# Kernel optimization log

Measured on AMD Instinct MI355X. Metric: run time of the kernel, lower is better.

## Reference

```python
import jax, jax.numpy as jnp
import numpy as np

B, T, D, H = 512, 1024, 64, 64     # batch, time, input_size, hidden_size
R = 4                              # number of reward heads
MH = 32                            # MLP hidden size


def setup_inputs() -> dict:
    key = jax.random.key(0)
    ks = jax.random.split(key, 16)
    s = lambda k, shape, scale=1.0: jax.random.normal(k, shape, dtype=jnp.float32) * scale
    inp = {
        "x": s(ks[0], (B, T, D)),
        # learned initial states (nn.Parameter randn(1,1,H) -> store as (H,))
        "h_init": s(ks[1], (H,)),
        "c_init": s(ks[2], (H,)),
        # LSTM params, PyTorch layout: W_ih (4H, D), W_hh (4H, H), gate order i,f,g,o
        "W_ih": s(ks[3], (4 * H, D), 1.0 / np.sqrt(H)),
        "W_hh": s(ks[4], (4 * H, H), 1.0 / np.sqrt(H)),
        "b_ih": s(ks[5], (4 * H,), 1.0 / np.sqrt(H)),
        "b_hh": s(ks[6], (4 * H,), 1.0 / np.sqrt(H)),
        # R stacked MLP heads: Linear(H,MH) -> ReLU -> Linear(MH,MH) -> ReLU -> Linear(MH,1)
        "W1": s(ks[7], (R, MH, H), 1.0 / np.sqrt(H)),
        "b1": s(ks[8], (R, MH), 1.0 / np.sqrt(H)),
        "W2": s(ks[9], (R, MH, MH), 1.0 / np.sqrt(MH)),
        "b2": s(ks[10], (R, MH), 1.0 / np.sqrt(MH)),
        "W3": s(ks[11], (R, 1, MH), 1.0 / np.sqrt(MH)),
        "b3": s(ks[12], (R, 1), 1.0 / np.sqrt(MH)),
    }
    return inp


def _lstm(x, h0, c0, W_ih, W_hh, b_ih, b_hh):
    # x: (B, T, D). Returns y: (B, T, H).
    Hh = h0.shape[-1]
    b = b_ih + b_hh                      # (4H,)
    # precompute input projections for all steps: (T, B, 4H)
    xg = jnp.einsum('btd,gd->tbg', x, W_ih) + b

    def step(carry, xg_t):
        h, c = carry                     # (B, H) each
        gates = xg_t + h @ W_hh.T        # (B, 4H)
        i, f, g, o = jnp.split(gates, 4, axis=-1)
        c = jax.nn.sigmoid(f) * c + jax.nn.sigmoid(i) * jnp.tanh(g)
        h = jax.nn.sigmoid(o) * jnp.tanh(c)
        return (h, c), h

    Bb = x.shape[0]
    h0b = jnp.broadcast_to(h0, (Bb, Hh))
    c0b = jnp.broadcast_to(c0, (Bb, Hh))
    _, ys = jax.lax.scan(step, (h0b, c0b), xg)   # ys: (T, B, H)
    return jnp.transpose(ys, (1, 0, 2))


def _heads(y, W1, b1, W2, b2, W3, b3):
    # y: (B, T, H) -> (R, B, T); all R heads computed in one batched einsum chain
    h1 = jax.nn.relu(jnp.einsum('bth,rmh->rbtm', y, W1) + b1[:, None, None, :])
    h2 = jax.nn.relu(jnp.einsum('rbtm,rnm->rbtn', h1, W2) + b2[:, None, None, :])
    out = jnp.einsum('rbtn,ron->rbto', h2, W3) + b3[:, None, None, :]
    return out[..., 0]                   # squeeze last dim -> (R, B, T)


def reference(x, h_init, c_init, W_ih, W_hh, b_ih, b_hh, W1, b1, W2, b2, W3, b3):
    y = _lstm(x, h_init, c_init, W_ih, W_hh, b_ih, b_hh)
    outs = _heads(y, W1, b1, W2, b2, W3, b3)   # (R, B, T); row r == rewards[r] head
    return (y, outs)
```

## Files before the change

kernel.cpp:

```cpp
#include <hip/hip_runtime.h>

#define BB 512
#define TT 1024
#define DD 64
#define HH 64
#define G4 256
#define RR 4
#define MHH 32
#define BT (BB * TT)
#define Y_SIZE (BB * TT * HH)

typedef _Float16 half8 __attribute__((ext_vector_type(8)));
typedef _Float16 half4 __attribute__((ext_vector_type(4)));
typedef float f32x4 __attribute__((ext_vector_type(4)));

#define MFMA16(a, b, c) __builtin_amdgcn_mfma_f32_16x16x32_f16((a), (b), (c), 0, 0, 0)

__device__ __forceinline__ float sigm(float x) {
    return __builtin_amdgcn_rcpf(1.0f + __expf(-x));
}
__device__ __forceinline__ float tanh_(float x) {
    return 1.0f - 2.0f * __builtin_amdgcn_rcpf(1.0f + __expf(2.0f * x));
}

__device__ __forceinline__ half8 cvt8(f32x4 a, f32x4 b) {
    half8 h;
    h[0] = (_Float16)a[0]; h[1] = (_Float16)a[1];
    h[2] = (_Float16)a[2]; h[3] = (_Float16)a[3];
    h[4] = (_Float16)b[0]; h[5] = (_Float16)b[1];
    h[6] = (_Float16)b[2]; h[7] = (_Float16)b[3];
    return h;
}

__global__ __launch_bounds__(256) void lstm_kernel(
    const float* __restrict__ x, const float* __restrict__ h_init,
    const float* __restrict__ c_init, const float* __restrict__ W_ih,
    const float* __restrict__ W_hh, const float* __restrict__ b_ih,
    const float* __restrict__ b_hh, float* __restrict__ y)
{
    __shared__ alignas(16) _Float16 xch[2][16][2][DD];
    __shared__ alignas(16) _Float16 hst[2][2][HH];

    const int tid  = threadIdx.x;
    const int wave = tid >> 6;
    const int lane = tid & 63;
    const int col  = lane & 15;
    const int quad = lane >> 4;
    const int sel  = (lane >> 3) & 1;
    const int r_act = lane >> 5;
    const int j    = (wave << 4) + col;
    const bool writer = ((lane >> 4) & 1) == 0;

    const int b0 = blockIdx.x * 2;

    half8 bf[4][4];
    float bias[4];
#pragma unroll
    for (int G = 0; G < 4; ++G) {
        const int n = (G << 6) + j;
        bias[G] = b_ih[n] + b_hh[n];
#pragma unroll
        for (int c = 0; c < 4; ++c) {
            const float* src = (c < 2) ? (W_ih + n * DD + c * 32 + quad * 8)
                                       : (W_hh + n * HH + (c - 2) * 32 + quad * 8);
            f32x4 w0 = *(const f32x4*)src;
            f32x4 w1 = *(const f32x4*)(src + 4);
            bf[G][c] = cvt8(w0, w1);
        }
    }

    float c_state = c_init[j];

    if (tid < 128) {
        const int rr = tid >> 6, jj = tid & 63;
        hst[0][rr][jj] = (_Float16)h_init[jj];
    }
    {
        const int ss = tid >> 4, rr = (tid >> 3) & 1, j0 = (tid & 7) << 3;
        const float* src = x + ((b0 + rr) * TT + ss) * DD + j0;
        f32x4 g0 = *(const f32x4*)src;
        f32x4 g1 = *(const f32x4*)(src + 4);
        *(half8*)&xch[0][ss][rr][j0] = cvt8(g0, g1);
    }
    __syncthreads();

    const int ss_pf = tid >> 4, rr_pf = (tid >> 3) & 1, j0_pf = (tid & 7) << 3;

    for (int ci = 0; ci < 64; ++ci) {
        const int buf = ci & 1;
        const bool pf = (ci + 1) < 64;
        f32x4 g0, g1;
        if (pf) {
            const float* src = x + ((b0 + rr_pf) * TT + ((ci + 1) << 4) + ss_pf) * DD + j0_pf;
            g0 = *(const f32x4*)src;
            g1 = *(const f32x4*)(src + 4);
        }
#pragma unroll
        for (int s = 0; s < 16; ++s) {
            const int t = (ci << 4) + s;
            const int p = s & 1;
            const _Float16* xrow = &xch[buf][s][sel][0];
            half8 a0 = *(const half8*)(xrow + quad * 8);
            half8 a1 = *(const half8*)(xrow + 32 + quad * 8);
            const _Float16* hrow = &hst[p][sel][0];
            half8 a2 = *(const half8*)(hrow + quad * 8);
            half8 a3 = *(const half8*)(hrow + 32 + quad * 8);

            f32x4 acc0 = {bias[0], bias[0], bias[0], bias[0]};
            f32x4 acc1 = {bias[1], bias[1], bias[1], bias[1]};
            f32x4 acc2 = {bias[2], bias[2], bias[2], bias[2]};
            f32x4 acc3 = {bias[3], bias[3], bias[3], bias[3]};
            acc0 = MFMA16(a0, bf[0][0], acc0); acc0 = MFMA16(a1, bf[0][1], acc0);
            acc0 = MFMA16(a2, bf[0][2], acc0); acc0 = MFMA16(a3, bf[0][3], acc0);
            acc1 = MFMA16(a0, bf[1][0], acc1); acc1 = MFMA16(a1, bf[1][1], acc1);
            acc1 = MFMA16(a2, bf[1][2], acc1); acc1 = MFMA16(a3, bf[1][3], acc1);
            acc2 = MFMA16(a0, bf[2][0], acc2); acc2 = MFMA16(a1, bf[2][1], acc2);
            acc2 = MFMA16(a2, bf[2][2], acc2); acc2 = MFMA16(a3, bf[2][3], acc2);
            acc3 = MFMA16(a0, bf[3][0], acc3); acc3 = MFMA16(a1, bf[3][1], acc3);
            acc3 = MFMA16(a2, bf[3][2], acc3); acc3 = MFMA16(a3, bf[3][3], acc3);

            const float si = sigm(acc0[0]);
            const float sf = sigm(acc1[0]);
            const float tg = tanh_(acc2[0]);
            const float so = sigm(acc3[0]);
            c_state = sf * c_state + si * tg;
            const float hv = so * tanh_(c_state);
            if (writer) {
                hst[p ^ 1][r_act][j] = (_Float16)hv;
                y[((b0 + r_act) * TT + t) * HH + j] = hv;
            }
            if (s == 15 && pf) {
                *(half8*)&xch[buf ^ 1][ss_pf][rr_pf][j0_pf] = cvt8(g0, g1);
            }
            __syncthreads();
        }
    }
}

__global__ __launch_bounds__(256) void heads_kernel(
    const float* __restrict__ y,
    const float* __restrict__ W1, const float* __restrict__ b1,
    const float* __restrict__ W2, const float* __restrict__ b2,
    const float* __restrict__ W3, const float* __restrict__ b3,
    float* __restrict__ outs)
{
    __shared__ alignas(16) _Float16 ybuf[64][72];
    __shared__ alignas(16) _Float16 h1buf[64][136];
    __shared__ alignas(16) _Float16 h2buf[64][136];

    const int tid  = threadIdx.x;
    const int wave = tid >> 6;
    const int lane = tid & 63;
    const int col  = lane & 15;
    const int quad = lane >> 4;
    const int arow = (wave << 4) + col;

    half8 w1f[8][2]; float bias1[8];
#pragma unroll
    for (int nt = 0; nt < 8; ++nt) {
        const int n = nt * 16 + col;
        bias1[nt] = b1[n];
#pragma unroll
        for (int c = 0; c < 2; ++c) {
            const float* src = W1 + n * 64 + c * 32 + quad * 8;
            w1f[nt][c] = cvt8(*(const f32x4*)src, *(const f32x4*)(src + 4));
        }
    }
    half8 w2f[8]; float bias2[8];
#pragma unroll
    for (int nt = 0; nt < 8; ++nt) {
        const int n = nt * 16 + col;
        bias2[nt] = b2[n];
        const float* src = W2 + n * 32 + quad * 8;
        w2f[nt] = cvt8(*(const f32x4*)src, *(const f32x4*)(src + 4));
    }
    const int hd3 = tid >> 6, row3 = tid & 63;
    float w3r[32];
#pragma unroll
    for (int i = 0; i < 32; i += 4) {
        f32x4 v = *(const f32x4*)(W3 + hd3 * 32 + i);
        w3r[i] = v[0]; w3r[i + 1] = v[1]; w3r[i + 2] = v[2]; w3r[i + 3] = v[3];
    }
    const float b3v = b3[hd3];

    for (int st = 0; st < 4; ++st) {
        const long base_row = (long)blockIdx.x * 256 + st * 64;
#pragma unroll
        for (int jj = 0; jj < 4; ++jj) {
            const int off = (jj * 256 + tid) * 4;
            const int row = off >> 6, cc = off & 63;
            f32x4 v = *(const f32x4*)(y + base_row * 64 + off);
            half4 hv = {(_Float16)v[0], (_Float16)v[1], (_Float16)v[2], (_Float16)v[3]};
            *(half4*)&ybuf[row][cc] = hv;
        }
        __syncthreads();

        half8 a0 = *(const half8*)&ybuf[arow][quad * 8];
        half8 a1 = *(const half8*)&ybuf[arow][32 + quad * 8];
#pragma unroll
        for (int nt = 0; nt < 8; ++nt) {
            f32x4 acc = {bias1[nt], bias1[nt], bias1[nt], bias1[nt]};
            acc = MFMA16(a0, w1f[nt][0], acc);
            acc = MFMA16(a1, w1f[nt][1], acc);
#pragma unroll
            for (int r = 0; r < 4; ++r) {
                float v = acc[r] > 0.0f ? acc[r] : 0.0f;
                h1buf[(wave << 4) + (quad << 2) + r][nt * 16 + col] = (_Float16)v;
            }
        }
        __syncthreads();

        half8 ah[4];
#pragma unroll
        for (int hd = 0; hd < 4; ++hd)
            ah[hd] = *(const half8*)&h1buf[arow][hd * 32 + quad * 8];
#pragma unroll
        for (int nt = 0; nt < 8; ++nt) {
            f32x4 acc = {bias2[nt], bias2[nt], bias2[nt], bias2[nt]};
            acc = MFMA16(ah[nt >> 1], w2f[nt], acc);
#pragma unroll
            for (int r = 0; r < 4; ++r) {
                float v = acc[r] > 0.0f ? acc[r] : 0.0f;
                h2buf[(wave << 4) + (quad << 2) + r][nt * 16 + col] = (_Float16)v;
            }
        }
        __syncthreads();

        float acc = b3v;
#pragma unroll
        for (int c = 0; c < 4; ++c) {
            half8 v = *(const half8*)&h2buf[row3][hd3 * 32 + c * 8];
#pragma unroll
            for (int u = 0; u < 8; ++u)
                acc = fmaf((float)v[u], w3r[c * 8 + u], acc);
        }
        outs[(long)hd3 * BT + base_row + row3] = acc;
        __syncthreads();
    }
}

extern "C" void kernel_launch(void* const* d_in, const int* in_sizes, int n_in,
                              void* d_out, int out_size, void* d_ws, size_t ws_size,
                              hipStream_t stream) {
    (void)in_sizes; (void)n_in; (void)out_size; (void)d_ws; (void)ws_size;
    const float* x      = (const float*)d_in[0];
    const float* h_init = (const float*)d_in[1];
    const float* c_init = (const float*)d_in[2];
    const float* W_ih   = (const float*)d_in[3];
    const float* W_hh   = (const float*)d_in[4];
    const float* b_ih   = (const float*)d_in[5];
    const float* b_hh   = (const float*)d_in[6];
    const float* W1     = (const float*)d_in[7];
    const float* b1     = (const float*)d_in[8];
    const float* W2     = (const float*)d_in[9];
    const float* b2     = (const float*)d_in[10];
    const float* W3     = (const float*)d_in[11];
    const float* b3     = (const float*)d_in[12];
    float* y    = (float*)d_out;
    float* outs = y + Y_SIZE;

    lstm_kernel<<<dim3(256), dim3(256), 0, stream>>>(x, h_init, c_init, W_ih, W_hh,
                                                     b_ih, b_hh, y);
    heads_kernel<<<dim3(2048), dim3(256), 0, stream>>>(y, W1, b1, W2, b2, W3, b3, outs);
}
```

Measured before the change: 569.7 us.

## Assign one batch row per LSTM block and interleave gate MFMA chains

The LSTM kernel now gives each block a single batch element instead of two, doubling the grid to 512 blocks so that all CUs on MI355X get work. Each block also carries half the per-step work along its sequential chain. The MFMA accumulation is reordered so the four gate accumulators are updated in an interleaved way, hiding MFMA dependency latency. Bias is preloaded as vectors used directly as the initial accumulator. The trade-off is that half of each MFMA's rows carry no useful data, and each block now does its per-step barrier and load work for only one sequence.

```diff
diff --git a/kernel.cpp b/kernel.cpp
--- a/kernel.cpp
+++ b/kernel.cpp
@@ -38,27 +38,26 @@
     const float* __restrict__ W_hh, const float* __restrict__ b_ih,
     const float* __restrict__ b_hh, float* __restrict__ y)
 {
-    __shared__ alignas(16) _Float16 xch[2][16][2][DD];
-    __shared__ alignas(16) _Float16 hst[2][2][HH];
+    __shared__ alignas(16) _Float16 xch[2][16][DD];
+    __shared__ alignas(16) _Float16 hst[2][HH];
 
     const int tid  = threadIdx.x;
     const int wave = tid >> 6;
     const int lane = tid & 63;
     const int col  = lane & 15;
     const int quad = lane >> 4;
-    const int sel  = (lane >> 3) & 1;
-    const int r_act = lane >> 5;
     const int j    = (wave << 4) + col;
-    const bool writer = ((lane >> 4) & 1) == 0;
-
-    const int b0 = blockIdx.x * 2;
+    const bool writer = (quad == 0);
+
+    const int b = blockIdx.x;
 
     half8 bf[4][4];
-    float bias[4];
+    f32x4 biasv[4];
 #pragma unroll
     for (int G = 0; G < 4; ++G) {
         const int n = (G << 6) + j;
-        bias[G] = b_ih[n] + b_hh[n];
+        const float bs = b_ih[n] + b_hh[n];
+        biasv[G][0] = bs; biasv[G][1] = bs; biasv[G][2] = bs; biasv[G][3] = bs;
 #pragma unroll
         for (int c = 0; c < 4; ++c) {
             const float* src = (c < 2) ? (W_ih + n * DD + c * 32 + quad * 8)
@@ -71,53 +70,45 @@
 
     float c_state = c_init[j];
 
-    if (tid < 128) {
-        const int rr = tid >> 6, jj = tid & 63;
-        hst[0][rr][jj] = (_Float16)h_init[jj];
-    }
+    if (tid < HH) hst[0][tid] = (_Float16)h_init[tid];
     {
-        const int ss = tid >> 4, rr = (tid >> 3) & 1, j0 = (tid & 7) << 3;
-        const float* src = x + ((b0 + rr) * TT + ss) * DD + j0;
-        f32x4 g0 = *(const f32x4*)src;
-        f32x4 g1 = *(const f32x4*)(src + 4);
-        *(half8*)&xch[0][ss][rr][j0] = cvt8(g0, g1);
+        const int ss = tid >> 4, j0 = (tid & 15) << 2;
+        f32x4 v = *(const f32x4*)(x + ((long)b * TT + ss) * DD + j0);
+        half4 hv = {(_Float16)v[0], (_Float16)v[1], (_Float16)v[2], (_Float16)v[3]};
+        *(half4*)&xch[0][ss][j0] = hv;
     }
     __syncthreads();
 
-    const int ss_pf = tid >> 4, rr_pf = (tid >> 3) & 1, j0_pf = (tid & 7) << 3;
+    const int ss_pf = tid >> 4, j0_pf = (tid & 15) << 2;
 
     for (int ci = 0; ci < 64; ++ci) {
         const int buf = ci & 1;
         const bool pf = (ci + 1) < 64;
-        f32x4 g0, g1;
+        f32x4 g0;
         if (pf) {
-            const float* src = x + ((b0 + rr_pf) * TT + ((ci + 1) << 4) + ss_pf) * DD + j0_pf;
-            g0 = *(const f32x4*)src;
-            g1 = *(const f32x4*)(src + 4);
+            g0 = *(const f32x4*)(x + ((long)b * TT + ((ci + 1) << 4) + ss_pf) * DD + j0_pf);
         }
 #pragma unroll
         for (int s = 0; s < 16; ++s) {
             const int t = (ci << 4) + s;
             const int p = s & 1;
-            const _Float16* xrow = &xch[buf][s][sel][0];
+            const _Float16* xrow = &xch[buf][s][0];
             half8 a0 = *(const half8*)(xrow + quad * 8);
             half8 a1 = *(const half8*)(xrow + 32 + quad * 8);
-            const _Float16* hrow = &hst[p][sel][0];
+            const _Float16* hrow = &hst[p][0];
             half8 a2 = *(const half8*)(hrow + quad * 8);
             half8 a3 = *(const half8*)(hrow + 32 + quad * 8);
 
-            f32x4 acc0 = {bias[0], bias[0], bias[0], bias[0]};
-            f32x4 acc1 = {bias[1], bias[1], bias[1], bias[1]};
-            f32x4 acc2 = {bias[2], bias[2], bias[2], bias[2]};
-            f32x4 acc3 = {bias[3], bias[3], bias[3], bias[3]};
-            acc0 = MFMA16(a0, bf[0][0], acc0); acc0 = MFMA16(a1, bf[0][1], acc0);
-            acc0 = MFMA16(a2, bf[0][2], acc0); acc0 = MFMA16(a3, bf[0][3], acc0);
-            acc1 = MFMA16(a0, bf[1][0], acc1); acc1 = MFMA16(a1, bf[1][1], acc1);
-            acc1 = MFMA16(a2, bf[1][2], acc1); acc1 = MFMA16(a3, bf[1][3], acc1);
-            acc2 = MFMA16(a0, bf[2][0], acc2); acc2 = MFMA16(a1, bf[2][1], acc2);
-            acc2 = MFMA16(a2, bf[2][2], acc2); acc2 = MFMA16(a3, bf[2][3], acc2);
-            acc3 = MFMA16(a0, bf[3][0], acc3); acc3 = MFMA16(a1, bf[3][1], acc3);
-            acc3 = MFMA16(a2, bf[3][2], acc3); acc3 = MFMA16(a3, bf[3][3], acc3);
+            f32x4 acc0 = MFMA16(a0, bf[0][0], biasv[0]);
+            f32x4 acc1 = MFMA16(a0, bf[1][0], biasv[1]);
+            f32x4 acc2 = MFMA16(a0, bf[2][0], biasv[2]);
+            f32x4 acc3 = MFMA16(a0, bf[3][0], biasv[3]);
+            acc0 = MFMA16(a1, bf[0][1], acc0); acc1 = MFMA16(a1, bf[1][1], acc1);
+            acc2 = MFMA16(a1, bf[2][1], acc2); acc3 = MFMA16(a1, bf[3][1], acc3);
+            acc0 = MFMA16(a2, bf[0][2], acc0); acc1 = MFMA16(a2, bf[1][2], acc1);
+            acc2 = MFMA16(a2, bf[2][2], acc2); acc3 = MFMA16(a2, bf[3][2], acc3);
+            acc0 = MFMA16(a3, bf[0][3], acc0); acc1 = MFMA16(a3, bf[1][3], acc1);
+            acc2 = MFMA16(a3, bf[2][3], acc2); acc3 = MFMA16(a3, bf[3][3], acc3);
 
             const float si = sigm(acc0[0]);
             const float sf = sigm(acc1[0]);
@@ -126,11 +117,13 @@
             c_state = sf * c_state + si * tg;
             const float hv = so * tanh_(c_state);
             if (writer) {
-                hst[p ^ 1][r_act][j] = (_Float16)hv;
-                y[((b0 + r_act) * TT + t) * HH + j] = hv;
+                hst[p ^ 1][j] = (_Float16)hv;
+                y[((long)b * TT + t) * HH + j] = hv;
             }
             if (s == 15 && pf) {
-                *(half8*)&xch[buf ^ 1][ss_pf][rr_pf][j0_pf] = cvt8(g0, g1);
+                half4 h4 = {(_Float16)g0[0], (_Float16)g0[1],
+                            (_Float16)g0[2], (_Float16)g0[3]};
+                *(half4*)&xch[buf ^ 1][ss_pf][j0_pf] = h4;
             }
             __syncthreads();
         }
@@ -259,7 +252,7 @@
     float* y    = (float*)d_out;
     float* outs = y + Y_SIZE;
 
-    lstm_kernel<<<dim3(256), dim3(256), 0, stream>>>(x, h_init, c_init, W_ih, W_hh,
+    lstm_kernel<<<dim3(512), dim3(256), 0, stream>>>(x, h_init, c_init, W_ih, W_hh,
                                                      b_ih, b_hh, y);
     heads_kernel<<<dim3(2048), dim3(256), 0, stream>>>(y, W1, b1, W2, b2, W3, b3, outs);
 }
```

Result: slower. 714.9 us (+25.5%).
